# Kernel tuning notes

Hardware: AMD Instinct MI355X
Metric: run time of the kernel (lower is better)

## Reference

```python
import jax, jax.numpy as jnp
import numpy as np

N_USERS = 100000
M_ITEMS = 50000
EMBED = 64
N_LAYERS = 3
NNZ = 2400000
BATCH = 8192


def setup_inputs() -> dict:
    key = jax.random.key(0)
    ks = jax.random.split(key, 8)
    user = jax.random.randint(ks[0], (BATCH,), 0, N_USERS)
    item_i = jax.random.randint(ks[1], (BATCH,), 0, M_ITEMS)
    item_j = jax.random.randint(ks[2], (BATCH,), 0, M_ITEMS)
    timestamp = jax.random.uniform(ks[3], (BATCH,), dtype=jnp.float32)
    # symmetric bipartite edge list: user->item and item->user halves
    half = NNZ // 2
    u = jax.random.randint(ks[4], (half,), 0, N_USERS)
    it = jax.random.randint(ks[5], (half,), 0, M_ITEMS) + N_USERS
    edge_src = jnp.concatenate([u, it])
    edge_dst = jnp.concatenate([it, u])
    v = jax.random.uniform(ks[6], (half,), dtype=jnp.float32)
    edge_vals = jnp.concatenate([v, v])  # symmetric normalized weights
    embed_user_0 = jax.random.normal(ks[7], (N_USERS, EMBED), dtype=jnp.float32) * 0.1
    embed_item_0 = jax.random.normal(jax.random.fold_in(key, 99), (M_ITEMS, EMBED), dtype=jnp.float32) * 0.1
    return {
        'user': user, 'item_i': item_i, 'item_j': item_j,
        'timestamp': timestamp, 'split_idx': 0,
        'edge_src': edge_src, 'edge_dst': edge_dst, 'edge_vals': edge_vals,
        'embed_user_0': embed_user_0, 'embed_item_0': embed_item_0,
    }


def reference(user, item_i, item_j, timestamp, split_idx,
              edge_src, edge_dst, edge_vals, embed_user_0, embed_item_0):
    N = N_USERS + M_ITEMS
    # LightGCN propagation: mean over layer-0..n_layers embeddings
    all_emb = jnp.concatenate([embed_user_0, embed_item_0], axis=0)  # [N, D]
    emb = all_emb
    emb_sum = all_emb
    for _ in range(N_LAYERS):
        # sparse.mm(Graph, emb): gather source features along edges, scale, segment-reduce
        emb = jax.ops.segment_sum(edge_vals[:, None] * emb[edge_dst], edge_src,
                                  num_segments=N)
        emb_sum = emb_sum + emb
    light_out = emb_sum / (N_LAYERS + 1)
    embed_user = light_out[:N_USERS]
    embed_item = light_out[N_USERS:]

    ue = embed_user[user]          # [B, D]
    ie = embed_item[item_i]        # [B, D]
    je = embed_item[item_j]        # [B, D]
    prediction_i = jnp.sum(ue * ie, axis=-1)
    prediction_j = jnp.sum(ue * je, axis=-1)

    # reg_loss uses layer-0 embeddings gathered at the batch indices
    u0 = embed_user_0[user]
    i0 = embed_item_0[item_i]
    j0 = embed_item_0[item_j]
    reg_loss = 0.5 * (jnp.sum(u0 * u0) + jnp.sum(i0 * i0) + jnp.sum(j0 * j0)) / user.shape[0]
    return prediction_i, prediction_j, reg_loss
```

## Files before the change

kernel.cpp:

```cpp
#include <hip/hip_runtime.h>
#include <hip/hip_fp16.h>

#define N_USERS 100000
#define M_ITEMS 50000
#define NNODES  (N_USERS + M_ITEMS)
#define EMBED   64
#define BATCH   8192

#define NU_E ((size_t)N_USERS * EMBED)
#define NE   ((size_t)NNODES * EMBED)

#define NPB    256
#define NBUCK  ((NNODES + NPB - 1) / NPB)
#define CAP    8192
#define CSTR   16
#define PBLK   512
#define PTILE  4688
#define BCAP   12288
#define PRED_BLOCKS ((BATCH * 64) / 256)

typedef unsigned int uint;

static __device__ __forceinline__ ushort f2bf(float f) {
    uint u = __float_as_uint(f);
    return (ushort)((u + 0x7fffu + ((u >> 16) & 1u)) >> 16);
}
static __device__ __forceinline__ float bf_lo(uint u) { return __uint_as_float(u << 16); }
static __device__ __forceinline__ float bf_hi(uint u) { return __uint_as_float(u & 0xffff0000u); }
static __device__ __forceinline__ float bfs(ushort u) { return __uint_as_float((uint)u << 16); }

static __device__ __forceinline__ int packe(int d, int fbits) {
    ushort h = __half_as_ushort(__float2half(__int_as_float(fbits)));
    return (int)(((uint)d << 15) | (uint)(h & 0x7fffu));
}
static __device__ __forceinline__ float unp_val(int p) {
    return __half2float(__ushort_as_half((ushort)(p & 0x7fff)));
}

__global__ void init_all(const float* __restrict__ eu, const float* __restrict__ ei,
                         ushort* __restrict__ E0, int* __restrict__ gcur) {
    if (blockIdx.x == 0) {
        for (int i = threadIdx.x; i < NBUCK; i += 1024) gcur[i * CSTR] = i * CAP;
        return;
    }
    size_t t = (size_t)(blockIdx.x - 1) * 1024 + threadIdx.x;
    const size_t nu4 = NU_E / 4;
    const size_t n4  = NE / 4;
    if (t >= n4) return;
    float4 v = (t < nu4) ? ((const float4*)eu)[t] : ((const float4*)ei)[t - nu4];
    ((ushort4*)E0)[t] = make_ushort4(f2bf(v.x), f2bf(v.y), f2bf(v.z), f2bf(v.w));
}

__global__ void __launch_bounds__(1024)
partition2(const int* __restrict__ src, const int* __restrict__ dst,
           const float* __restrict__ vals, int* __restrict__ gcur,
           int2* __restrict__ ebuf, int nnz) {
    __shared__ int2 data[PTILE];
    __shared__ int  cnt[NBUCK];
    __shared__ int  cur[NBUCK];
    __shared__ int  gbase[NBUCK];
    __shared__ int  s[1024];
    const int blk = blockIdx.x;
    const int tid = threadIdx.x;
    const int base = blk * PTILE;
    const int end  = min(base + PTILE, nnz);

    for (int i = tid; i < NBUCK; i += 1024) cnt[i] = 0;
    __syncthreads();
    for (int i = base + tid; i < end; i += 1024)
        atomicAdd(&cnt[src[i] >> 8], 1);
    __syncthreads();
    if (tid < NBUCK && cnt[tid] > 0)
        gbase[tid] = atomicAdd(&gcur[tid * CSTR], cnt[tid]);
    s[tid] = (tid < NBUCK) ? cnt[tid] : 0;
    __syncthreads();
    for (int off = 1; off < 1024; off <<= 1) {
        int t = (tid >= off) ? s[tid - off] : 0;
        __syncthreads();
        s[tid] += t;
        __syncthreads();
    }
    if (tid < NBUCK) cur[tid] = (tid > 0) ? s[tid - 1] : 0;
    __syncthreads();
    for (int i = base + tid; i < end; i += 1024) {
        int sv = src[i];
        int d  = dst[i];
        float v = vals[i];
        if (d >= N_USERS) d -= N_USERS;
        int p = atomicAdd(&cur[sv >> 8], 1);
        data[p] = make_int2((sv & 255) | (d << 8), __float_as_int(v));
    }
    __syncthreads();
    int grp = tid >> 4, lane16 = tid & 15;
    for (int b = grp; b < NBUCK; b += 64) {
        int c = cnt[b];
        if (c == 0) continue;
        int lbeg = (b > 0) ? s[b - 1] : 0;
        int gb = gbase[b];
        for (int j = lane16; j < c; j += 16)
            ebuf[gb + j] = data[lbeg + j];
    }
}

__global__ void __launch_bounds__(1024)
bucket_sort_perm(const int* __restrict__ gcur, const int2* __restrict__ ebuf,
                 int2* __restrict__ offs2, int* __restrict__ ep,
                 int* __restrict__ perm) {
    __shared__ int data[BCAP];
    __shared__ int cnt[256], sc[256], cur[256], dsc[256];
    int b   = blockIdx.x;
    int tid = threadIdx.x;
    int beg = b * CAP;
    int end = gcur[b * CSTR];
    int blen = end - beg;
    if (tid < 256) cnt[tid] = 0;
    __syncthreads();
    for (int i = beg + tid; i < end; i += 1024)
        atomicAdd(&cnt[ebuf[i].x & 255], 1);
    __syncthreads();
    if (tid < 256) sc[tid] = cnt[tid];
    __syncthreads();
    for (int off = 1; off < 256; off <<= 1) {
        int t = (tid >= off && tid < 256) ? sc[tid - off] : 0;
        __syncthreads();
        if (tid < 256) sc[tid] += t;
        __syncthreads();
    }
    if (tid < 256) {
        int lbase = (tid > 0) ? sc[tid - 1] : 0;
        int node = b * NPB + tid;
        if (node < NNODES) offs2[node] = make_int2(beg + lbase, cnt[tid]);
        cur[tid] = lbase;
    }
    __syncthreads();
    if (blen <= BCAP) {
        for (int i = beg + tid; i < end; i += 1024) {
            int2 e = ebuf[i];
            int p = atomicAdd(&cur[e.x & 255], 1);
            data[p] = packe(e.x >> 8, e.y);
        }
        __syncthreads();
        for (int i = tid; i < blen; i += 1024)
            ep[beg + i] = data[i];
    } else {
        for (int i = beg + tid; i < end; i += 1024) {
            int2 e = ebuf[i];
            int p = atomicAdd(&cur[e.x & 255], 1);
            ep[beg + p] = packe(e.x >> 8, e.y);
        }
    }
    __syncthreads();
    if (tid < 256) sc[tid] = 0;
    __syncthreads();
    int nodeCount = min(NNODES - b * NPB, NPB);
    int bin = 0;
    if (tid < nodeCount) {
        bin = min(cnt[tid], 255);
        atomicAdd(&sc[bin], 1);
    }
    __syncthreads();
    if (tid < 256) dsc[tid] = sc[tid];
    __syncthreads();
    for (int off = 1; off < 256; off <<= 1) {
        int t = (tid >= off && tid < 256) ? dsc[tid - off] : 0;
        __syncthreads();
        if (tid < 256) dsc[tid] += t;
        __syncthreads();
    }
    if (tid < 256) cur[tid] = b * NPB + ((tid > 0) ? dsc[tid - 1] : 0);
    __syncthreads();
    if (tid < nodeCount) {
        int rank = atomicAdd(&cur[bin], 1);
        perm[rank] = b * NPB + tid;
    }
}

__global__ void gather_E(const int2* __restrict__ offs2, const int* __restrict__ ep,
                         const int* __restrict__ perm,
                         const ushort* __restrict__ Eprev, ushort* __restrict__ Enext) {
    int t = blockIdx.x * blockDim.x + threadIdx.x;
    int wave = t >> 6;
    int lane = t & 63;
    int g = lane >> 3;
    int q = lane & 7;
    int ln = wave * 8 + g;
    bool valid = ln < NNODES;
    int node = valid ? perm[ln] : 0;
    int2 od = valid ? offs2[node] : make_int2(0, 0);
    int start = od.x;
    int deg   = od.y;
    const uint4* other = (const uint4*)(Eprev + (node < N_USERS ? NU_E : 0));
    int lastIdx = max(start + deg - 1, 0);

    int md = deg;
    #pragma unroll
    for (int off = 8; off <= 32; off <<= 1) md = max(md, __shfl_xor(md, off));

    float a0=0.f,a1=0.f,a2=0.f,a3=0.f,a4=0.f,a5=0.f,a6=0.f,a7=0.f;
    for (int k = 0; k < md; k += 8) {
        int e[8];
        uint4 r[8];
        #pragma unroll
        for (int c = 0; c < 8; ++c) {
            int idx = (k + c < deg) ? start + k + c : lastIdx;
            e[c] = ep[idx];
            if (k + c >= deg) e[c] = 0;
        }
        #pragma unroll
        for (int c = 0; c < 8; ++c)
            r[c] = other[(size_t)(((uint)e[c]) >> 15) * 8 + q];
        #pragma unroll
        for (int c = 0; c < 8; ++c) {
            float v = unp_val(e[c]);
            a0 = fmaf(v, bf_lo(r[c].x), a0);  a1 = fmaf(v, bf_hi(r[c].x), a1);
            a2 = fmaf(v, bf_lo(r[c].y), a2);  a3 = fmaf(v, bf_hi(r[c].y), a3);
            a4 = fmaf(v, bf_lo(r[c].z), a4);  a5 = fmaf(v, bf_hi(r[c].z), a5);
            a6 = fmaf(v, bf_lo(r[c].w), a6);  a7 = fmaf(v, bf_hi(r[c].w), a7);
        }
    }

    if (!valid) return;
    uint4 o;
    o.x = (uint)f2bf(a0) | ((uint)f2bf(a1) << 16);
    o.y = (uint)f2bf(a2) | ((uint)f2bf(a3) << 16);
    o.z = (uint)f2bf(a4) | ((uint)f2bf(a5) << 16);
    o.w = (uint)f2bf(a6) | ((uint)f2bf(a7) << 16);
    ((uint4*)Enext)[(size_t)node * 8 + q] = o;
}

__global__ void predict_kernel(const int* __restrict__ user, const int* __restrict__ item_i,
                               const int* __restrict__ item_j,
                               const ushort* __restrict__ E0, const ushort* __restrict__ E1,
                               const ushort* __restrict__ E2, const ushort* __restrict__ E3,
                               const float* __restrict__ eu0, const float* __restrict__ ei0,
                               float* __restrict__ out, float* __restrict__ rbuf) {
    __shared__ float rpart[4];
    int t = blockIdx.x * blockDim.x + threadIdx.x;
    int b = t >> 6;
    int d = t & 63;
    int wv = threadIdx.x >> 6;
    float pi = 0.f, pj = 0.f, r = 0.f;
    if (b < BATCH) {
        size_t ru = (size_t)user[b] * EMBED + d;
        size_t ri = ((size_t)N_USERS + item_i[b]) * EMBED + d;
        size_t rj = ((size_t)N_USERS + item_j[b]) * EMBED + d;
        float ue = bfs(E0[ru]) + bfs(E1[ru]) + bfs(E2[ru]) + bfs(E3[ru]);
        float ie = bfs(E0[ri]) + bfs(E1[ri]) + bfs(E2[ri]) + bfs(E3[ri]);
        float je = bfs(E0[rj]) + bfs(E1[rj]) + bfs(E2[rj]) + bfs(E3[rj]);
        pi = ue * ie;
        pj = ue * je;
        float u0 = eu0[(size_t)user[b] * EMBED + d];
        float i0 = ei0[(size_t)item_i[b] * EMBED + d];
        float j0 = ei0[(size_t)item_j[b] * EMBED + d];
        r = u0 * u0 + i0 * i0 + j0 * j0;
    }
    #pragma unroll
    for (int off = 32; off > 0; off >>= 1) {
        pi += __shfl_down(pi, off);
        pj += __shfl_down(pj, off);
        r  += __shfl_down(r,  off);
    }
    if (d == 0 && b < BATCH) {
        out[b]         = pi * (1.0f / 16.0f);
        out[BATCH + b] = pj * (1.0f / 16.0f);
        rpart[wv] = r;
    }
    __syncthreads();
    if (threadIdx.x == 0)
        rbuf[blockIdx.x] = rpart[0] + rpart[1] + rpart[2] + rpart[3];
}

__global__ void finalize_reg(const float* __restrict__ rbuf, float* __restrict__ out) {
    __shared__ float lds[4];
    int tid = threadIdx.x;
    float s = 0.f;
    for (int i = tid; i < PRED_BLOCKS; i += 256) s += rbuf[i];
    #pragma unroll
    for (int off = 32; off > 0; off >>= 1) s += __shfl_down(s, off);
    if ((tid & 63) == 0) lds[tid >> 6] = s;
    __syncthreads();
    if (tid == 0)
        out[2 * BATCH] = (lds[0] + lds[1] + lds[2] + lds[3]) * (0.5f / (float)BATCH);
}

extern "C" void kernel_launch(void* const* d_in, const int* in_sizes, int n_in,
                              void* d_out, int out_size, void* d_ws, size_t ws_size,
                              hipStream_t stream) {
    const int*   user      = (const int*)  d_in[0];
    const int*   item_i    = (const int*)  d_in[1];
    const int*   item_j    = (const int*)  d_in[2];
    const int*   edge_src  = (const int*)  d_in[5];
    const int*   edge_dst  = (const int*)  d_in[6];
    const float* edge_vals = (const float*)d_in[7];
    const float* eu0       = (const float*)d_in[8];
    const float* ei0       = (const float*)d_in[9];
    const int    nnz       = in_sizes[5];

    float* out = (float*)d_out;

    ushort* E0    = (ushort*)d_ws;
    ushort* E1    = E0 + NE;
    ushort* E2    = E1 + NE;
    ushort* E3    = E2 + NE;
    int*    ep    = (int*)(E3 + NE);
    int2*   offs2 = (int2*)(ep + (size_t)NBUCK * CAP);
    int*    gcur  = (int*)(offs2 + NNODES);
    int*    perm  = gcur + NBUCK * CSTR;
    float*  rbuf  = (float*)(perm + NNODES);
    int2*   ebuf  = (int2*)E1;

    const int initBlocks = (int)((NE / 4 + 1023) / 1024);

    init_all<<<1 + initBlocks, 1024, 0, stream>>>(eu0, ei0, E0, gcur);
    partition2<<<PBLK, 1024, 0, stream>>>(edge_src, edge_dst, edge_vals,
                                          gcur, ebuf, nnz);
    bucket_sort_perm<<<NBUCK, 1024, 0, stream>>>(gcur, ebuf, offs2, ep, perm);
    const int gblocks = (int)((((NNODES + 7) / 8) * 64 + 255) / 256);
    gather_E<<<gblocks, 256, 0, stream>>>(offs2, ep, perm, E0, E1);
    gather_E<<<gblocks, 256, 0, stream>>>(offs2, ep, perm, E1, E2);
    gather_E<<<gblocks, 256, 0, stream>>>(offs2, ep, perm, E2, E3);
    predict_kernel<<<PRED_BLOCKS, 256, 0, stream>>>(
        user, item_i, item_j, E0, E1, E2, E3, eu0, ei0, out, rbuf);
    finalize_reg<<<1, 256, 0, stream>>>(rbuf, out);
}
```

Baseline: 309.9 us.

## Replace two-pass bucket sort with global-atomic histogram, scan, and scatter CSR build

Builds the CSR edge layout with a per-node global atomic degree histogram, a two-level prefix scan, and a direct atomic scatter into the packed edge array. This replaces the shared-memory bucket partition and per-bucket local sort. The goal is to drop the intermediate ebuf pass and the fixed-capacity buckets. The cost is heavy global atomic contention on random node indices and more kernel launches. Edge order within a node also becomes nondeterministic.

```diff
diff --git a/kernel.cpp b/kernel.cpp
--- a/kernel.cpp
+++ b/kernel.cpp
@@ -12,11 +12,9 @@
 
 #define NPB    256
 #define NBUCK  ((NNODES + NPB - 1) / NPB)
-#define CAP    8192
-#define CSTR   16
-#define PBLK   512
-#define PTILE  4688
-#define BCAP   12288
+#define SCHUNK 2048
+#define SNB    ((NNODES + SCHUNK - 1) / SCHUNK)
+#define ZB     37
 #define PRED_BLOCKS ((BATCH * 64) / 256)
 
 typedef unsigned int uint;
@@ -38,12 +36,18 @@
 }
 
 __global__ void init_all(const float* __restrict__ eu, const float* __restrict__ ei,
-                         ushort* __restrict__ E0, int* __restrict__ gcur) {
-    if (blockIdx.x == 0) {
-        for (int i = threadIdx.x; i < NBUCK; i += 1024) gcur[i * CSTR] = i * CAP;
+                         ushort* __restrict__ E0, int* __restrict__ offs) {
+    if (blockIdx.x < ZB) {
+        int idx = (blockIdx.x * 1024 + threadIdx.x) * 4;
+        if (idx + 3 < NNODES + 1) {
+            *(int4*)(offs + idx) = make_int4(0, 0, 0, 0);
+        } else {
+            for (int k = 0; k < 4; ++k)
+                if (idx + k < NNODES + 1) offs[idx + k] = 0;
+        }
         return;
     }
-    size_t t = (size_t)(blockIdx.x - 1) * 1024 + threadIdx.x;
+    size_t t = (size_t)(blockIdx.x - ZB) * 1024 + threadIdx.x;
     const size_t nu4 = NU_E / 4;
     const size_t n4  = NE / 4;
     if (t >= n4) return;
@@ -51,127 +55,106 @@
     ((ushort4*)E0)[t] = make_ushort4(f2bf(v.x), f2bf(v.y), f2bf(v.z), f2bf(v.w));
 }
 
-__global__ void __launch_bounds__(1024)
-partition2(const int* __restrict__ src, const int* __restrict__ dst,
-           const float* __restrict__ vals, int* __restrict__ gcur,
-           int2* __restrict__ ebuf, int nnz) {
-    __shared__ int2 data[PTILE];
-    __shared__ int  cnt[NBUCK];
-    __shared__ int  cur[NBUCK];
-    __shared__ int  gbase[NBUCK];
-    __shared__ int  s[1024];
-    const int blk = blockIdx.x;
+__global__ void hist_deg(const int* __restrict__ src, int* __restrict__ offs, int nnz) {
+    int i = blockIdx.x * blockDim.x + threadIdx.x;
+    int stride = gridDim.x * blockDim.x;
+    for (; i < nnz; i += stride)
+        atomicAdd(&offs[src[i]], 1);
+}
+
+__global__ void scan_local(int* __restrict__ h, int* __restrict__ bsum, int n) {
+    __shared__ int lds[256];
     const int tid = threadIdx.x;
-    const int base = blk * PTILE;
-    const int end  = min(base + PTILE, nnz);
-
-    for (int i = tid; i < NBUCK; i += 1024) cnt[i] = 0;
-    __syncthreads();
-    for (int i = base + tid; i < end; i += 1024)
-        atomicAdd(&cnt[src[i] >> 8], 1);
-    __syncthreads();
-    if (tid < NBUCK && cnt[tid] > 0)
-        gbase[tid] = atomicAdd(&gcur[tid * CSTR], cnt[tid]);
-    s[tid] = (tid < NBUCK) ? cnt[tid] : 0;
-    __syncthreads();
-    for (int off = 1; off < 1024; off <<= 1) {
-        int t = (tid >= off) ? s[tid - off] : 0;
-        __syncthreads();
-        s[tid] += t;
-        __syncthreads();
-    }
-    if (tid < NBUCK) cur[tid] = (tid > 0) ? s[tid - 1] : 0;
-    __syncthreads();
-    for (int i = base + tid; i < end; i += 1024) {
+    const int base = blockIdx.x * SCHUNK + tid * 8;
+    int v[8]; int s = 0;
+    #pragma unroll
+    for (int c = 0; c < 8; ++c) { v[c] = (base + c < n) ? h[base + c] : 0; s += v[c]; }
+    lds[tid] = s;
+    __syncthreads();
+    for (int off = 1; off < 256; off <<= 1) {
+        int t = (tid >= off) ? lds[tid - off] : 0;
+        __syncthreads();
+        lds[tid] += t;
+        __syncthreads();
+    }
+    if (tid == 255) bsum[blockIdx.x] = lds[255];
+    int run = (tid > 0) ? lds[tid - 1] : 0;
+    #pragma unroll
+    for (int c = 0; c < 8; ++c) {
+        int t = v[c];
+        if (base + c < n) h[base + c] = run;
+        run += t;
+    }
+}
+
+__global__ void scan_add2(int* __restrict__ h, const int* __restrict__ bsum,
+                          int* __restrict__ cur, int n, int nblk, int nnz) {
+    __shared__ int lds[256];
+    int tid = threadIdx.x;
+    if (tid < 256) lds[tid] = (tid < nblk) ? bsum[tid] : 0;
+    __syncthreads();
+    for (int off = 1; off < 256; off <<= 1) {
+        int t = (tid >= off && tid < 256) ? lds[tid - off] : 0;
+        __syncthreads();
+        if (tid < 256) lds[tid] += t;
+        __syncthreads();
+    }
+    int prefix = (blockIdx.x > 0) ? lds[blockIdx.x - 1] : 0;
+    int lim = min(blockIdx.x * SCHUNK + SCHUNK, n);
+    for (int i = blockIdx.x * SCHUNK + tid; i < lim; i += 1024) {
+        int v = h[i] + prefix;
+        h[i] = v;
+        cur[i] = v;
+    }
+    if (blockIdx.x == 0 && tid == 0) h[n] = nnz;
+}
+
+__global__ void scatter_ep(const int* __restrict__ src, const int* __restrict__ dst,
+                           const float* __restrict__ vals,
+                           int* __restrict__ cur, int* __restrict__ ep, int nnz) {
+    int i = blockIdx.x * blockDim.x + threadIdx.x;
+    int stride = gridDim.x * blockDim.x;
+    for (; i < nnz; i += stride) {
         int sv = src[i];
         int d  = dst[i];
         float v = vals[i];
         if (d >= N_USERS) d -= N_USERS;
-        int p = atomicAdd(&cur[sv >> 8], 1);
-        data[p] = make_int2((sv & 255) | (d << 8), __float_as_int(v));
-    }
-    __syncthreads();
-    int grp = tid >> 4, lane16 = tid & 15;
-    for (int b = grp; b < NBUCK; b += 64) {
-        int c = cnt[b];
-        if (c == 0) continue;
-        int lbeg = (b > 0) ? s[b - 1] : 0;
-        int gb = gbase[b];
-        for (int j = lane16; j < c; j += 16)
-            ebuf[gb + j] = data[lbeg + j];
-    }
-}
-
-__global__ void __launch_bounds__(1024)
-bucket_sort_perm(const int* __restrict__ gcur, const int2* __restrict__ ebuf,
-                 int2* __restrict__ offs2, int* __restrict__ ep,
-                 int* __restrict__ perm) {
-    __shared__ int data[BCAP];
-    __shared__ int cnt[256], sc[256], cur[256], dsc[256];
-    int b   = blockIdx.x;
-    int tid = threadIdx.x;
-    int beg = b * CAP;
-    int end = gcur[b * CSTR];
-    int blen = end - beg;
-    if (tid < 256) cnt[tid] = 0;
-    __syncthreads();
-    for (int i = beg + tid; i < end; i += 1024)
-        atomicAdd(&cnt[ebuf[i].x & 255], 1);
-    __syncthreads();
-    if (tid < 256) sc[tid] = cnt[tid];
+        int p = atomicAdd(&cur[sv], 1);
+        ep[p] = packe(d, __float_as_int(v));
+    }
+}
+
+__global__ void __launch_bounds__(256)
+perm_offs2(const int* __restrict__ offs, int2* __restrict__ offs2,
+           int* __restrict__ perm) {
+    __shared__ int sc[256], dsc[256], cur[256];
+    int b = blockIdx.x, tid = threadIdx.x;
+    int node = b * NPB + tid;
+    int nodeCount = min(NNODES - b * NPB, NPB);
+    int deg = 0;
+    if (tid < nodeCount) {
+        int st = offs[node];
+        deg = offs[node + 1] - st;
+        offs2[node] = make_int2(st, deg);
+    }
+    int bin = min(deg, 255);
+    sc[tid] = 0;
+    __syncthreads();
+    if (tid < nodeCount) atomicAdd(&sc[bin], 1);
+    __syncthreads();
+    dsc[tid] = sc[tid];
     __syncthreads();
     for (int off = 1; off < 256; off <<= 1) {
-        int t = (tid >= off && tid < 256) ? sc[tid - off] : 0;
-        __syncthreads();
-        if (tid < 256) sc[tid] += t;
-        __syncthreads();
-    }
-    if (tid < 256) {
-        int lbase = (tid > 0) ? sc[tid - 1] : 0;
-        int node = b * NPB + tid;
-        if (node < NNODES) offs2[node] = make_int2(beg + lbase, cnt[tid]);
-        cur[tid] = lbase;
-    }
-    __syncthreads();
-    if (blen <= BCAP) {
-        for (int i = beg + tid; i < end; i += 1024) {
-            int2 e = ebuf[i];
-            int p = atomicAdd(&cur[e.x & 255], 1);
-            data[p] = packe(e.x >> 8, e.y);
-        }
-        __syncthreads();
-        for (int i = tid; i < blen; i += 1024)
-            ep[beg + i] = data[i];
-    } else {
-        for (int i = beg + tid; i < end; i += 1024) {
-            int2 e = ebuf[i];
-            int p = atomicAdd(&cur[e.x & 255], 1);
-            ep[beg + p] = packe(e.x >> 8, e.y);
-        }
-    }
-    __syncthreads();
-    if (tid < 256) sc[tid] = 0;
-    __syncthreads();
-    int nodeCount = min(NNODES - b * NPB, NPB);
-    int bin = 0;
-    if (tid < nodeCount) {
-        bin = min(cnt[tid], 255);
-        atomicAdd(&sc[bin], 1);
-    }
-    __syncthreads();
-    if (tid < 256) dsc[tid] = sc[tid];
-    __syncthreads();
-    for (int off = 1; off < 256; off <<= 1) {
-        int t = (tid >= off && tid < 256) ? dsc[tid - off] : 0;
-        __syncthreads();
-        if (tid < 256) dsc[tid] += t;
-        __syncthreads();
-    }
-    if (tid < 256) cur[tid] = b * NPB + ((tid > 0) ? dsc[tid - 1] : 0);
+        int t = (tid >= off) ? dsc[tid - off] : 0;
+        __syncthreads();
+        dsc[tid] += t;
+        __syncthreads();
+    }
+    cur[tid] = b * NPB + ((tid > 0) ? dsc[tid - 1] : 0);
     __syncthreads();
     if (tid < nodeCount) {
         int rank = atomicAdd(&cur[bin], 1);
-        perm[rank] = b * NPB + tid;
+        perm[rank] = node;
     }
 }
 
@@ -303,18 +286,21 @@
     ushort* E2    = E1 + NE;
     ushort* E3    = E2 + NE;
     int*    ep    = (int*)(E3 + NE);
-    int2*   offs2 = (int2*)(ep + (size_t)NBUCK * CAP);
-    int*    gcur  = (int*)(offs2 + NNODES);
-    int*    perm  = gcur + NBUCK * CSTR;
-    float*  rbuf  = (float*)(perm + NNODES);
-    int2*   ebuf  = (int2*)E1;
+    int*    offs  = ep + nnz;
+    int*    cur   = offs + NNODES + 2;
+    int2*   offs2 = (int2*)(cur + NNODES);
+    int*    perm  = (int*)(offs2 + NNODES);
+    int*    bsum  = perm + NNODES;
+    float*  rbuf  = (float*)(bsum + 256);
 
     const int initBlocks = (int)((NE / 4 + 1023) / 1024);
 
-    init_all<<<1 + initBlocks, 1024, 0, stream>>>(eu0, ei0, E0, gcur);
-    partition2<<<PBLK, 1024, 0, stream>>>(edge_src, edge_dst, edge_vals,
-                                          gcur, ebuf, nnz);
-    bucket_sort_perm<<<NBUCK, 1024, 0, stream>>>(gcur, ebuf, offs2, ep, perm);
+    init_all<<<ZB + initBlocks, 1024, 0, stream>>>(eu0, ei0, E0, offs);
+    hist_deg<<<2048, 256, 0, stream>>>(edge_src, offs, nnz);
+    scan_local<<<SNB, 256, 0, stream>>>(offs, bsum, NNODES);
+    scan_add2<<<SNB, 1024, 0, stream>>>(offs, bsum, cur, NNODES, SNB, nnz);
+    scatter_ep<<<2048, 256, 0, stream>>>(edge_src, edge_dst, edge_vals, cur, ep, nnz);
+    perm_offs2<<<NBUCK, 256, 0, stream>>>(offs, offs2, perm);
     const int gblocks = (int)((((NNODES + 7) / 8) * 64 + 255) / 256);
     gather_E<<<gblocks, 256, 0, stream>>>(offs2, ep, perm, E0, E1);
     gather_E<<<gblocks, 256, 0, stream>>>(offs2, ep, perm, E1, E2);
```

New measurement: 502.0 us. 1.62x slower.
